# Kernel tuning notes

Hardware: AMD Instinct MI355X
Metric: run time of the kernel (lower is better)

The kernel has to match this reference:

```python
import jax, jax.numpy as jnp
import numpy as np
import math

ALPHA = 2.0  # mnist_para.alpha (standard atan-surrogate sharpness)
TAU = 0.5    # membrane leak factor

@jax.custom_vjp
def spike_fn(u):
    # Heaviside step forward, atan surrogate gradient backward
    return (u >= 0.0).astype(u.dtype)

def _spike_fwd(u):
    return spike_fn(u), u

def _spike_bwd(u, g):
    surr = ALPHA / 2.0 / (1.0 + jnp.square(ALPHA * math.pi / 2.0 * u))
    return (surr * g,)

spike_fn.defvjp(_spike_fwd, _spike_bwd)

def setup_inputs() -> dict:
    key = jax.random.key(0)
    k1, k2 = jax.random.split(key)
    B, T, N = 64, 100, 4096
    x = jax.random.normal(k1, (B, T, N), dtype=jnp.float32)
    # thresh = heterogeneity * randn / 100 + thresh_base  (base 0.5, het 1.0)
    thresh = 0.5 + jax.random.normal(k2, (N,), dtype=jnp.float32) / 100.0
    return {"x": x, "thresh": thresh}

def reference(x, thresh):
    # x: [B, T, N]; scan over T with sequential membrane state
    def step(mem, x_t):
        mem = mem * TAU + x_t                      # leaky integrate
        spk = spike_fn(mem - thresh)               # fire
        mem = (1.0 - spk) * mem                    # hard reset
        return mem, spk
    xs = jnp.swapaxes(x, 0, 1)                     # [T, B, N]
    mem0 = jnp.zeros_like(xs[0])
    _, spikes = jax.lax.scan(step, mem0, xs)       # spikes: [T, B, N]
    return jnp.swapaxes(spikes, 0, 1)              # [B, T, N]
```

## Files before the change

### kernel.cpp

```cpp
#include <hip/hip_runtime.h>


constexpr int T = 100;
constexpr int N = 4096;
constexpr int B = 64;
constexpr float TAU = 0.5f;

__device__ __forceinline__ void lif_step(float& mem, float x, float th, float& spk) {
    float m = mem * TAU + x;
    float u = m - th;
    bool s = (u >= 0.0f);
    spk = s ? 1.0f : 0.0f;
    mem = s ? 0.0f : m;
}

__global__ __launch_bounds__(256) void lif_fwd(const float4* __restrict__ x,
                                               const float4* __restrict__ thresh4,
                                               float4* __restrict__ out) {
    const int idx = blockIdx.x * 256 + threadIdx.x;
    const int n4  = idx & (N / 4 - 1);
    const int b   = idx >> 10;

    const float4 th = thresh4[n4];
    float4 mem = make_float4(0.f, 0.f, 0.f, 0.f);

    const long row = (long)b * T * (N / 4) + n4;
    const float4* xp = x + row;
    float4* op = out + row;

    #pragma unroll 4
    for (int t = 0; t < T; ++t) {
        const float4 xv = xp[(long)t * (N / 4)];
        float4 spk;
        lif_step(mem.x, xv.x, th.x, spk.x);
        lif_step(mem.y, xv.y, th.y, spk.y);
        lif_step(mem.z, xv.z, th.z, spk.z);
        lif_step(mem.w, xv.w, th.w, spk.w);
        op[(long)t * (N / 4)] = spk;
    }
}

extern "C" void kernel_launch(void* const* d_in, const int* in_sizes, int n_in,
                              void* d_out, int out_size, void* d_ws, size_t ws_size,
                              hipStream_t stream) {
    const float4* x  = (const float4*)d_in[0];
    const float4* th = (const float4*)d_in[1];
    float4* out = (float4*)d_out;

    const int total = B * N / 4;
    lif_fwd<<<total / 256, 256, 0, stream>>>(x, th, out);
}
```

Measured before the change: 36.61 us.

## Double-buffer time-step loads in registers and halve per-thread vector width

Each thread now handles two neurons (float2) instead of four, which doubles the thread count. Inputs for ten time steps are prefetched into a register buffer while the previous ten-step group is computed, so loads are issued ahead of the sequential membrane recurrence. The goal is more memory-level parallelism to hide global load latency in this bandwidth-bound scan. The cost is higher register use and 8-byte rather than 16-byte transactions per access.

```diff
diff --git a/kernel.cpp b/kernel.cpp
--- a/kernel.cpp
+++ b/kernel.cpp
@@ -1,52 +1,82 @@
 #include <hip/hip_runtime.h>
 
+
+typedef float v2f __attribute__((ext_vector_type(2)));
 
 constexpr int T = 100;
 constexpr int N = 4096;
 constexpr int B = 64;
-constexpr float TAU = 0.5f;
+constexpr int U = 10;
+constexpr int NG = T / U;
+constexpr int S = N / 2;
 
-__device__ __forceinline__ void lif_step(float& mem, float x, float th, float& spk) {
-    float m = mem * TAU + x;
-    float u = m - th;
-    bool s = (u >= 0.0f);
-    spk = s ? 1.0f : 0.0f;
-    mem = s ? 0.0f : m;
-}
+__global__ __launch_bounds__(256) void lif_fwd(const v2f* __restrict__ x,
+                                               const v2f* __restrict__ th2,
+                                               v2f* __restrict__ out) {
+    const int idx = blockIdx.x * 256 + threadIdx.x;
+    const int n2  = idx & (S - 1);
+    const int b   = idx >> 11;
 
-__global__ __launch_bounds__(256) void lif_fwd(const float4* __restrict__ x,
-                                               const float4* __restrict__ thresh4,
-                                               float4* __restrict__ out) {
-    const int idx = blockIdx.x * 256 + threadIdx.x;
-    const int n4  = idx & (N / 4 - 1);
-    const int b   = idx >> 10;
+    const v2f th = th2[n2];
+    float m0 = 0.f, m1 = 0.f;
 
-    const float4 th = thresh4[n4];
-    float4 mem = make_float4(0.f, 0.f, 0.f, 0.f);
+    const long row = (long)b * T * S + n2;
+    const v2f* __restrict__ xp = x + row;
+    v2f* __restrict__ op = out + row;
 
-    const long row = (long)b * T * (N / 4) + n4;
-    const float4* xp = x + row;
-    float4* op = out + row;
+    v2f bufA[U], bufB[U];
 
-    #pragma unroll 4
-    for (int t = 0; t < T; ++t) {
-        const float4 xv = xp[(long)t * (N / 4)];
-        float4 spk;
-        lif_step(mem.x, xv.x, th.x, spk.x);
-        lif_step(mem.y, xv.y, th.y, spk.y);
-        lif_step(mem.z, xv.z, th.z, spk.z);
-        lif_step(mem.w, xv.w, th.w, spk.w);
-        op[(long)t * (N / 4)] = spk;
+    #pragma unroll
+    for (int u = 0; u < U; ++u) bufA[u] = xp[(long)u * S];
+
+    for (int g = 0; g < NG; g += 2) {
+        #pragma unroll
+        for (int u = 0; u < U; ++u) bufB[u] = xp[(long)((g + 1) * U + u) * S];
+
+        #pragma unroll
+        for (int u = 0; u < U; ++u) {
+            const v2f xv = bufA[u];
+            const float a = m0 * 0.5f + xv.x;
+            const float c = m1 * 0.5f + xv.y;
+            const bool s0 = (a - th.x) >= 0.0f;
+            const bool s1 = (c - th.y) >= 0.0f;
+            v2f spk;
+            spk.x = s0 ? 1.0f : 0.0f;
+            spk.y = s1 ? 1.0f : 0.0f;
+            m0 = s0 ? 0.0f : a;
+            m1 = s1 ? 0.0f : c;
+            op[(long)(g * U + u) * S] = spk;
+        }
+
+        if (g + 2 < NG) {
+            #pragma unroll
+            for (int u = 0; u < U; ++u) bufA[u] = xp[(long)((g + 2) * U + u) * S];
+        }
+
+        #pragma unroll
+        for (int u = 0; u < U; ++u) {
+            const v2f xv = bufB[u];
+            const float a = m0 * 0.5f + xv.x;
+            const float c = m1 * 0.5f + xv.y;
+            const bool s0 = (a - th.x) >= 0.0f;
+            const bool s1 = (c - th.y) >= 0.0f;
+            v2f spk;
+            spk.x = s0 ? 1.0f : 0.0f;
+            spk.y = s1 ? 1.0f : 0.0f;
+            m0 = s0 ? 0.0f : a;
+            m1 = s1 ? 0.0f : c;
+            op[(long)((g + 1) * U + u) * S] = spk;
+        }
     }
 }
 
 extern "C" void kernel_launch(void* const* d_in, const int* in_sizes, int n_in,
                               void* d_out, int out_size, void* d_ws, size_t ws_size,
                               hipStream_t stream) {
-    const float4* x  = (const float4*)d_in[0];
-    const float4* th = (const float4*)d_in[1];
-    float4* out = (float4*)d_out;
+    const v2f* x  = (const v2f*)d_in[0];
+    const v2f* th = (const v2f*)d_in[1];
+    v2f* out = (v2f*)d_out;
 
-    const int total = B * N / 4;
+    const int total = B * N / 2;
     lif_fwd<<<total / 256, 256, 0, stream>>>(x, th, out);
 }
```

After: 35.41 us. 1.03x faster.

## Use scalar per-thread neurons with double-buffered register prefetch of timesteps

Applied to the files above, without the earlier changes.

Switches from float4 per thread to one float per thread, giving four times as many threads (1024 blocks instead of 256). Each thread loads timesteps in groups of ten into register buffers and prefetches the next group while computing the current one. The aim is more memory-level parallelism and better hiding of the serial recurrence's load latency. In exchange it uses narrower 4-byte accesses and more registers per thread.

```diff
diff --git a/kernel.cpp b/kernel.cpp
--- a/kernel.cpp
+++ b/kernel.cpp
@@ -4,49 +4,62 @@
 constexpr int T = 100;
 constexpr int N = 4096;
 constexpr int B = 64;
-constexpr float TAU = 0.5f;
+constexpr int U = 10;
+constexpr int NG = T / U;
 
-__device__ __forceinline__ void lif_step(float& mem, float x, float th, float& spk) {
-    float m = mem * TAU + x;
-    float u = m - th;
-    bool s = (u >= 0.0f);
-    spk = s ? 1.0f : 0.0f;
-    mem = s ? 0.0f : m;
-}
+__global__ __launch_bounds__(256) void lif_fwd(const float* __restrict__ x,
+                                               const float* __restrict__ thresh,
+                                               float* __restrict__ out) {
+    const int idx = blockIdx.x * 256 + threadIdx.x;
+    const int n   = idx & (N - 1);
+    const int b   = idx >> 12;
 
-__global__ __launch_bounds__(256) void lif_fwd(const float4* __restrict__ x,
-                                               const float4* __restrict__ thresh4,
-                                               float4* __restrict__ out) {
-    const int idx = blockIdx.x * 256 + threadIdx.x;
-    const int n4  = idx & (N / 4 - 1);
-    const int b   = idx >> 10;
+    const float th = thresh[n];
+    float mem = 0.f;
 
-    const float4 th = thresh4[n4];
-    float4 mem = make_float4(0.f, 0.f, 0.f, 0.f);
+    const long row = (long)b * T * N + n;
+    const float* __restrict__ xp = x + row;
+    float* __restrict__ op = out + row;
 
-    const long row = (long)b * T * (N / 4) + n4;
-    const float4* xp = x + row;
-    float4* op = out + row;
+    float bufA[U], bufB[U];
 
-    #pragma unroll 4
-    for (int t = 0; t < T; ++t) {
-        const float4 xv = xp[(long)t * (N / 4)];
-        float4 spk;
-        lif_step(mem.x, xv.x, th.x, spk.x);
-        lif_step(mem.y, xv.y, th.y, spk.y);
-        lif_step(mem.z, xv.z, th.z, spk.z);
-        lif_step(mem.w, xv.w, th.w, spk.w);
-        op[(long)t * (N / 4)] = spk;
+    #pragma unroll
+    for (int u = 0; u < U; ++u) bufA[u] = xp[(long)u * N];
+
+    for (int g = 0; g < NG; g += 2) {
+        #pragma unroll
+        for (int u = 0; u < U; ++u) bufB[u] = xp[(long)((g + 1) * U + u) * N];
+
+        #pragma unroll
+        for (int u = 0; u < U; ++u) {
+            const float m = mem * 0.5f + bufA[u];
+            const bool s = (m - th) >= 0.0f;
+            op[(long)(g * U + u) * N] = s ? 1.0f : 0.0f;
+            mem = s ? 0.0f : m;
+        }
+
+        if (g + 2 < NG) {
+            #pragma unroll
+            for (int u = 0; u < U; ++u) bufA[u] = xp[(long)((g + 2) * U + u) * N];
+        }
+
+        #pragma unroll
+        for (int u = 0; u < U; ++u) {
+            const float m = mem * 0.5f + bufB[u];
+            const bool s = (m - th) >= 0.0f;
+            op[(long)((g + 1) * U + u) * N] = s ? 1.0f : 0.0f;
+            mem = s ? 0.0f : m;
+        }
     }
 }
 
 extern "C" void kernel_launch(void* const* d_in, const int* in_sizes, int n_in,
                               void* d_out, int out_size, void* d_ws, size_t ws_size,
                               hipStream_t stream) {
-    const float4* x  = (const float4*)d_in[0];
-    const float4* th = (const float4*)d_in[1];
-    float4* out = (float4*)d_out;
+    const float* x  = (const float*)d_in[0];
+    const float* th = (const float*)d_in[1];
+    float* out = (float*)d_out;
 
-    const int total = B * N / 4;
+    const int total = B * N;
     lif_fwd<<<total / 256, 256, 0, stream>>>(x, th, out);
 }
```

Result: faster. 35.75 us (-2.4%).
